# Kernel tuning notes

Hardware: AMD Instinct MI355X
Metric: run time of the kernel (lower is better)

## Reference

```python
import jax, jax.numpy as jnp
import numpy as np

B, N, D = 4, 1024, 1024   # batch, seq (x and context must match), model dim
H, DH = 16, 64            # heads, dim_head; inner_dim = H*DH = 1024
INNER = H * DH
EPS = 1e-5


def setup_inputs() -> dict:
    key = jax.random.key(0)
    ks = jax.random.split(key, 12)
    s = 0.02
    return {
        "x": jax.random.normal(ks[0], (B, N, D), dtype=jnp.float32),
        "context": jax.random.normal(ks[1], (B, N, D), dtype=jnp.float32),
        # weights stored as [in, out] (torch Linear weight transposed)
        "W_qk": jax.random.normal(ks[2], (D, INNER), dtype=jnp.float32) * s,
        "W_cqk": jax.random.normal(ks[3], (D, INNER), dtype=jnp.float32) * s,
        "W_v": jax.random.normal(ks[4], (D, INNER), dtype=jnp.float32) * s,
        "W_cv": jax.random.normal(ks[5], (D, INNER), dtype=jnp.float32) * s,
        "W_out": jax.random.normal(ks[6], (INNER, D), dtype=jnp.float32) * s,
        "b_out": jax.random.normal(ks[7], (D,), dtype=jnp.float32) * s,
        "W_cout": jax.random.normal(ks[8], (INNER, D), dtype=jnp.float32) * s,
        "b_cout": jax.random.normal(ks[9], (D,), dtype=jnp.float32) * s,
        "gamma": jnp.ones((D,), dtype=jnp.float32),
        "beta": jnp.zeros((D,), dtype=jnp.float32),
    }


def _split_heads(t):  # [b, n, h*d] -> [b, h, n, d]
    b, n, _ = t.shape
    return t.reshape(b, n, H, DH).transpose(0, 2, 1, 3)


def _merge_heads(t):  # [b, h, n, d] -> [b, n, h*d]
    b, h, n, d = t.shape
    return t.transpose(0, 2, 1, 3).reshape(b, n, h * d)


def _layernorm(y, gamma, beta):
    mu = jnp.mean(y, axis=-1, keepdims=True)
    var = jnp.var(y, axis=-1, keepdims=True)
    return gamma * (y - mu) * jax.lax.rsqrt(var + EPS) + beta


def reference(x, context, W_qk, W_cqk, W_v, W_cv, W_out, b_out, W_cout, b_cout, gamma, beta):
    scale = DH ** -0.5
    res = x + context                       # residual (requires identical shapes)
    # prenorm=False -> identity norms; dropout=0; talking_heads=False -> identity
    qk = _split_heads(x @ W_qk)             # [b,h,i,d]
    v = _split_heads(x @ W_v)               # [b,h,i,d]
    cqk = _split_heads(context @ W_cqk)     # [b,h,j,d]
    cv = _split_heads(context @ W_cv)       # [b,h,j,d]

    sim = jnp.einsum('bhid,bhjd->bhij', qk, cqk) * scale  # shared similarity
    attn = jax.nn.softmax(sim, axis=-1)      # row softmax (x attends to context)
    context_attn = jax.nn.softmax(sim, axis=-2)  # column softmax (context attends to x)

    out = jnp.einsum('bhij,bhjd->bhid', attn, cv)          # [b,h,i,d]
    context_out = jnp.einsum('bhji,bhjd->bhid', context_attn, v)  # [b,h,i,d]

    out = _merge_heads(out) @ W_out + b_out
    context_out = _merge_heads(context_out) @ W_cout + b_cout
    return _layernorm(out + context_out, gamma, beta) + res
```

## Files before the change

### kernel.cpp

```cpp
#include <hip/hip_runtime.h>
#include <hip/hip_bf16.h>

typedef unsigned short u16;
typedef __bf16 bf16x8 __attribute__((ext_vector_type(8)));
typedef float   f32x4 __attribute__((ext_vector_type(4)));
typedef u16     u16x8 __attribute__((ext_vector_type(8)));
typedef u16     u16x4 __attribute__((ext_vector_type(4)));

#define DEV static __device__ __forceinline__

DEV float bf2f(u16 b) { unsigned int u = ((unsigned int)b) << 16; return __builtin_bit_cast(float, u); }
DEV u16   f2bf(float f) { return __builtin_bit_cast(u16, (__bf16)f); }
DEV bf16x8 ldb(const u16* p) { return __builtin_bit_cast(bf16x8, *(const u16x8*)p); }

DEV f32x4 mfma_bf16(bf16x8 a, bf16x8 b, f32x4 c) {
  return __builtin_amdgcn_mfma_f32_16x16x32_bf16(a, b, c, 0, 0, 0);
}

DEV void gl16(const u16* g, u16* l) {
  __builtin_amdgcn_global_load_lds((const __attribute__((address_space(1))) unsigned int*)g,
                                   (__attribute__((address_space(3))) unsigned int*)l,
                                   16, 0, 0);
}

#define BAR_VM4() asm volatile("s_waitcnt vmcnt(4)\ns_barrier" ::: "memory")
#define BAR_VM0() asm volatile("s_waitcnt vmcnt(0)\ns_barrier" ::: "memory")
#define BAR_LG()  asm volatile("s_waitcnt lgkmcnt(0)\ns_barrier" ::: "memory")

__global__ __launch_bounds__(256) void detect_dtype(const u16* x, int* flag) {
  int tid = threadIdx.x;
  u16 lo = x[tid * 2];
  float v = bf2f(lo);
  float av = fabsf(v);
  bool plaus = (av > 1e-4f && av < 50.f);
  __shared__ int cnt;
  if (tid == 0) cnt = 0;
  __syncthreads();
  if (plaus) atomicAdd(&cnt, 1);
  __syncthreads();
  if (tid == 0) *flag = (cnt >= 128) ? 1 : 0;
}

struct Cv2 { const void* s[2]; u16* d[2]; };
__global__ __launch_bounds__(256) void convert_big(Cv2 p, const int* flagp) {
  int fl = *flagp;
  const void* src = p.s[blockIdx.z];
  u16* dst = p.d[blockIdx.z];
  size_t i = ((size_t)blockIdx.x * 256 + threadIdx.x) * 8;
  if (fl) {
    *(u16x8*)(dst + i) = *(const u16x8*)((const u16*)src + i);
  } else {
    const float* s = (const float*)src + i;
    u16x8 o;
#pragma unroll
    for (int k = 0; k < 8; ++k) o[k] = f2bf(s[k]);
    *(u16x8*)(dst + i) = o;
  }
}

struct Sm4 { const void* s[4]; u16* d[4]; };
__global__ __launch_bounds__(256) void convert_smalls(Sm4 p, const int* flagp) {
  int fl = *flagp;
  const void* src = p.s[blockIdx.x];
  u16* dst = p.d[blockIdx.x];
  int i = threadIdx.x * 4;
#pragma unroll
  for (int k = 0; k < 4; ++k)
    dst[i + k] = fl ? ((const u16*)src)[i + k] : f2bf(((const float*)src)[i + k]);
}

struct T6 { const void* s[6]; u16* d[6]; };

__global__ __launch_bounds__(256) void transpose6(T6 t, const int* flagp) {
  int fl = *flagp;
  __shared__ u16 tile[32][33];
  const void* src = t.s[blockIdx.z];
  u16* dst = t.d[blockIdx.z];
  int x0 = blockIdx.x * 32, y0 = blockIdx.y * 32;
  int tx = threadIdx.x & 31, ty = threadIdx.x >> 5;
#pragma unroll
  for (int i = 0; i < 32; i += 8) {
    size_t idx = (size_t)(y0 + ty + i) * 1024 + x0 + tx;
    tile[ty + i][tx] = fl ? ((const u16*)src)[idx] : f2bf(((const float*)src)[idx]);
  }
  __syncthreads();
#pragma unroll
  for (int i = 0; i < 32; i += 8)
    dst[(size_t)(x0 + ty + i) * 1024 + y0 + tx] = tile[tx][ty + i];
}

struct Proj4 { const u16* A[4]; const u16* Bt[4]; u16* C[4]; int mode[4]; };

__global__ __launch_bounds__(256) void gemm_proj(Proj4 p) {
  const int K = 1024, Nn = 1024;
  const u16* A  = p.A[blockIdx.z];
  const u16* Bt = p.Bt[blockIdx.z];
  u16* C = p.C[blockIdx.z];
  int mode = p.mode[blockIdx.z];

  __shared__ __align__(16) u16 As[2][128 * 32];
  __shared__ __align__(16) u16 Bs[2][128 * 32];

  int tid = threadIdx.x, lane = tid & 63, w = tid >> 6;
  int wm = w & 1, wn = w >> 1;
  int q4 = lane >> 4, c = lane & 15;

  int bid = blockIdx.y * 8 + blockIdx.x;
  int wg  = (bid & 7) * 32 + (bid >> 3);
  int m0 = (wg >> 3) * 128, n0 = (wg & 7) * 128;

  int r0 = w * 32 + (lane >> 2);
  int cc = (lane & 3) ^ ((lane >> 3) & 3);
  const u16* pA0 = A  + (size_t)(m0 + r0) * K + cc * 8;
  const u16* pB0 = Bt + (size_t)(n0 + r0) * K + cc * 8;
  int qs = (q4 ^ ((c >> 1) & 3)) * 8;

  f32x4 acc[4][4] = {};

#define STAGE_P(buf, koff)                                        \
  { gl16(pA0 + (koff),          As[buf] + w * 1024);              \
    gl16(pA0 + 16 * K + (koff), As[buf] + w * 1024 + 512);        \
    gl16(pB0 + (koff),          Bs[buf] + w * 1024);              \
    gl16(pB0 + 16 * K + (koff), Bs[buf] + w * 1024 + 512); }

#define COMP_P(buf)                                               \
  { bf16x8 af[4], bfr[4];                                         \
    _Pragma("unroll") for (int i = 0; i < 4; ++i)                 \
      af[i]  = ldb(As[buf] + (wm * 64 + i * 16 + c) * 32 + qs);   \
    _Pragma("unroll") for (int j = 0; j < 4; ++j)                 \
      bfr[j] = ldb(Bs[buf] + (wn * 64 + j * 16 + c) * 32 + qs);   \
    _Pragma("unroll") for (int i = 0; i < 4; ++i)                 \
      _Pragma("unroll") for (int j = 0; j < 4; ++j)               \
        acc[i][j] = mfma_bf16(af[i], bfr[j], acc[i][j]); }

  STAGE_P(0, 0);
  for (int t = 0; t < 30; t += 2) {
    STAGE_P(1, (t + 1) * 32);
    BAR_VM4();
    COMP_P(0);
    BAR_LG();
    STAGE_P(0, (t + 2) * 32);
    BAR_VM4();
    COMP_P(1);
    BAR_LG();
  }
  STAGE_P(1, 31 * 32);
  BAR_VM4();
  COMP_P(0);
  BAR_LG();
  BAR_VM0();
  COMP_P(1);
#undef STAGE_P
#undef COMP_P

  if (mode == 0) {
#pragma unroll
    for (int i = 0; i < 4; ++i) {
      int mrow = m0 + wm * 64 + i * 16 + q4 * 4;
#pragma unroll
      for (int j = 0; j < 4; ++j) {
        int col = n0 + wn * 64 + j * 16 + c;
#pragma unroll
        for (int r = 0; r < 4; ++r)
          C[(size_t)(mrow + r) * Nn + col] = f2bf(acc[i][j][r]);
      }
    }
  } else {
    int bidx = m0 >> 10;
#pragma unroll
    for (int i = 0; i < 4; ++i) {
      int mrow = m0 + wm * 64 + i * 16 + q4 * 4;
      int jj = mrow & 1023;
#pragma unroll
      for (int j = 0; j < 4; ++j) {
        int col = n0 + wn * 64 + j * 16 + c;
        int h = col >> 6, dh = col & 63;
        u16x4 pk;
#pragma unroll
        for (int r = 0; r < 4; ++r) pk[r] = f2bf(acc[i][j][r]);
        *(u16x4*)(C + ((size_t)((bidx * 16 + h) * 64 + dh)) * 1024 + jj) = pk;
      }
    }
  }
}

__global__ __launch_bounds__(256) void flash_attn(const u16* Q, const u16* Kg,
                                                  const u16* Vt, u16* O) {
  int bh = blockIdx.y; int b = bh >> 4, h = bh & 15;
  int i0 = blockIdx.x * 128;
  int tid = threadIdx.x, lane = tid & 63, w = tid >> 6;
  int q4 = lane >> 4, c = lane & 15;

  __shared__ __align__(16) u16 Ks[64 * 72];
  __shared__ __align__(16) u16 Vs[64 * 72];
  __shared__ __align__(16) u16 Ps[4][2][16 * 72];

  bf16x8 qf[2][2];
#pragma unroll
  for (int g = 0; g < 2; ++g) {
    const size_t qoff = ((size_t)(b * 1024 + i0 + g * 64 + w * 16 + c)) * 1024 + h * 64 + q4 * 8;
    qf[g][0] = ldb(Q + qoff);
    qf[g][1] = ldb(Q + qoff + 32);
  }

  f32x4 of[2][4] = {};
  f32x4 lacc[2] = {};
  bf16x8 ones;
#pragma unroll
  for (int k = 0; k < 8; ++k) ones[k] = (__bf16)1.0f;

  int jr = tid >> 2, seg = (tid & 3) * 16;
  const u16* krow_base = Kg + ((size_t)(b * 1024 + jr)) * 1024 + h * 64 + seg;
  const u16* vrow_base = Vt + ((size_t)((b * 16 + h) * 64 + jr)) * 1024 + seg;
  const float scale = 0.125f;

  u16x8 kv0 = *(const u16x8*)(krow_base);
  u16x8 kv1 = *(const u16x8*)(krow_base + 8);
  u16x8 vv0 = *(const u16x8*)(vrow_base);
  u16x8 vv1 = *(const u16x8*)(vrow_base + 8);

  for (int j0 = 0; j0 < 1024; j0 += 64) {
    __syncthreads();
    *(u16x8*)(Ks + jr * 72 + seg)     = kv0;
    *(u16x8*)(Ks + jr * 72 + seg + 8) = kv1;
    *(u16x8*)(Vs + jr * 72 + seg)     = vv0;
    *(u16x8*)(Vs + jr * 72 + seg + 8) = vv1;
    __syncthreads();

    if (j0 + 64 < 1024) {
      const u16* ks = krow_base + (size_t)(j0 + 64) * 1024;
      kv0 = *(const u16x8*)(ks);
      kv1 = *(const u16x8*)(ks + 8);
      const u16* vs = vrow_base + j0 + 64;
      vv0 = *(const u16x8*)(vs);
      vv1 = *(const u16x8*)(vs + 8);
    }

    f32x4 sf[2][4] = {};
    __builtin_amdgcn_s_setprio(1);
#pragma unroll
    for (int jc = 0; jc < 4; ++jc) {
      bf16x8 k0f = ldb(Ks + (jc * 16 + c) * 72 + q4 * 8);
      bf16x8 k1f = ldb(Ks + (jc * 16 + c) * 72 + 32 + q4 * 8);
#pragma unroll
      for (int g = 0; g < 2; ++g) {
        sf[g][jc] = mfma_bf16(k0f, qf[g][0], sf[g][jc]);
        sf[g][jc] = mfma_bf16(k1f, qf[g][1], sf[g][jc]);
      }
    }
    __builtin_amdgcn_s_setprio(0);

#pragma unroll
    for (int g = 0; g < 2; ++g)
#pragma unroll
      for (int jc = 0; jc < 4; ++jc) {
        u16x4 pk;
#pragma unroll
        for (int r = 0; r < 4; ++r) {
          float s = fminf(fmaxf(sf[g][jc][r] * scale, -60.f), 60.f);
          pk[r] = f2bf(__expf(s));
        }
        *(u16x4*)(Ps[w][g] + c * 72 + jc * 16 + q4 * 4) = pk;
      }

    asm volatile("s_waitcnt lgkmcnt(0)" ::: "memory");

    bf16x8 pf[2][2];
#pragma unroll
    for (int g = 0; g < 2; ++g) {
      pf[g][0] = ldb(Ps[w][g] + c * 72 + q4 * 8);
      pf[g][1] = ldb(Ps[w][g] + c * 72 + 32 + q4 * 8);
      lacc[g] = mfma_bf16(pf[g][0], ones, lacc[g]);
      lacc[g] = mfma_bf16(pf[g][1], ones, lacc[g]);
    }

    __builtin_amdgcn_s_setprio(1);
#pragma unroll
    for (int dc = 0; dc < 4; ++dc) {
      bf16x8 v0f = ldb(Vs + (dc * 16 + c) * 72 + q4 * 8);
      bf16x8 v1f = ldb(Vs + (dc * 16 + c) * 72 + 32 + q4 * 8);
#pragma unroll
      for (int g = 0; g < 2; ++g) {
        of[g][dc] = mfma_bf16(pf[g][0], v0f, of[g][dc]);
        of[g][dc] = mfma_bf16(pf[g][1], v1f, of[g][dc]);
      }
    }
    __builtin_amdgcn_s_setprio(0);
  }

#pragma unroll
  for (int g = 0; g < 2; ++g) {
    float inv[4];
#pragma unroll
    for (int r = 0; r < 4; ++r) inv[r] = 1.0f / lacc[g][r];
#pragma unroll
    for (int dc = 0; dc < 4; ++dc) {
      int col = h * 64 + dc * 16 + c;
#pragma unroll
      for (int r = 0; r < 4; ++r) {
        int irow = i0 + g * 64 + w * 16 + q4 * 4 + r;
        O[((size_t)(b * 1024 + irow)) * 1024 + col] = f2bf(of[g][dc][r] * inv[r]);
      }
    }
  }
}

__global__ __launch_bounds__(256) void gemm_final(const u16* A1, const u16* B1t,
                                                  const u16* A2, const u16* B2t,
                                                  const u16* b1, const u16* b2,
                                                  float* Y) {
  const int K = 1024, Nn = 1024;
  __shared__ __align__(16) u16 As[2][128 * 32];
  __shared__ __align__(16) u16 Bs[2][128 * 32];

  int tid = threadIdx.x, lane = tid & 63, w = tid >> 6;
  int wm = w & 1, wn = w >> 1;
  int q4 = lane >> 4, c = lane & 15;

  int bid = blockIdx.y * 8 + blockIdx.x;
  int wg  = (bid & 7) * 32 + (bid >> 3);
  int m0 = (wg >> 3) * 128, n0 = (wg & 7) * 128;

  int r0 = w * 32 + (lane >> 2);
  int cc = (lane & 3) ^ ((lane >> 3) & 3);
  const u16* A1p = A1  + (size_t)(m0 + r0) * K + cc * 8;
  const u16* A2p = A2  + (size_t)(m0 + r0) * K + cc * 8;
  const u16* B1p = B1t + (size_t)(n0 + r0) * K + cc * 8;
  const u16* B2p = B2t + (size_t)(n0 + r0) * K + cc * 8;
  int qs = (q4 ^ ((c >> 1) & 3)) * 8;

  f32x4 acc[4][4] = {};

#define STAGE_F(buf, kk)                                          \
  { const u16* Ap = ((kk) < 32) ? A1p : A2p;                      \
    const u16* Bp = ((kk) < 32) ? B1p : B2p;                      \
    int k0_ = ((kk) & 31) * 32;                                   \
    gl16(Ap + k0_,          As[buf] + w * 1024);                  \
    gl16(Ap + 16 * K + k0_, As[buf] + w * 1024 + 512);            \
    gl16(Bp + k0_,          Bs[buf] + w * 1024);                  \
    gl16(Bp + 16 * K + k0_, Bs[buf] + w * 1024 + 512); }

#define COMP_F(buf)                                               \
  { bf16x8 af[4], bfr[4];                                         \
    _Pragma("unroll") for (int i = 0; i < 4; ++i)                 \
      af[i]  = ldb(As[buf] + (wm * 64 + i * 16 + c) * 32 + qs);   \
    _Pragma("unroll") for (int j = 0; j < 4; ++j)                 \
      bfr[j] = ldb(Bs[buf] + (wn * 64 + j * 16 + c) * 32 + qs);   \
    _Pragma("unroll") for (int i = 0; i < 4; ++i)                 \
      _Pragma("unroll") for (int j = 0; j < 4; ++j)               \
        acc[i][j] = mfma_bf16(af[i], bfr[j], acc[i][j]); }

  STAGE_F(0, 0);
  for (int t = 0; t < 62; t += 2) {
    STAGE_F(1, t + 1);
    BAR_VM4();
    COMP_F(0);
    BAR_LG();
    STAGE_F(0, t + 2);
    BAR_VM4();
    COMP_F(1);
    BAR_LG();
  }
  STAGE_F(1, 63);
  BAR_VM4();
  COMP_F(0);
  BAR_LG();
  BAR_VM0();
  COMP_F(1);
#undef STAGE_F
#undef COMP_F

#pragma unroll
  for (int i = 0; i < 4; ++i) {
    int mrow = m0 + wm * 64 + i * 16 + q4 * 4;
#pragma unroll
    for (int j = 0; j < 4; ++j) {
      int col = n0 + wn * 64 + j * 16 + c;
      float bias = bf2f(b1[col]) + bf2f(b2[col]);
#pragma unroll
      for (int r = 0; r < 4; ++r)
        Y[(size_t)(mrow + r) * Nn + col] = acc[i][j][r] + bias;
    }
  }
}

__global__ __launch_bounds__(256) void ln_res(const float* Y, const u16* gamma, const u16* beta,
                                              const u16* x, const u16* ctx, void* out,
                                              const int* flagp) {
  int fl = *flagp;
  int row = blockIdx.x;
  int tid = threadIdx.x;
  const float* y = Y + (size_t)row * 1024;
  float4 v = *(const float4*)(y + tid * 4);
  float s  = v.x + v.y + v.z + v.w;
  float s2 = v.x * v.x + v.y * v.y + v.z * v.z + v.w * v.w;
#pragma unroll
  for (int off = 1; off < 64; off <<= 1) { s += __shfl_xor(s, off); s2 += __shfl_xor(s2, off); }
  __shared__ float red[8];
  int w = tid >> 6, lane = tid & 63;
  if (lane == 0) { red[w] = s; red[w + 4] = s2; }
  __syncthreads();
  float S  = red[0] + red[1] + red[2] + red[3];
  float S2 = red[4] + red[5] + red[6] + red[7];
  float mu  = S * (1.0f / 1024.0f);
  float var = S2 * (1.0f / 1024.0f) - mu * mu;
  float rs = rsqrtf(var + 1e-5f);
  size_t base = (size_t)row * 1024 + tid * 4;
  u16x4 gv = *(const u16x4*)(gamma + tid * 4);
  u16x4 bv = *(const u16x4*)(beta + tid * 4);
  u16x4 xv = *(const u16x4*)(x + base);
  u16x4 cv = *(const u16x4*)(ctx + base);
  float vv[4] = {v.x, v.y, v.z, v.w};
  float o[4];
#pragma unroll
  for (int k = 0; k < 4; ++k)
    o[k] = bf2f(gv[k]) * (vv[k] - mu) * rs + bf2f(bv[k]) + bf2f(xv[k]) + bf2f(cv[k]);
  if (fl) {
    u16x4 ov;
#pragma unroll
    for (int k = 0; k < 4; ++k) ov[k] = f2bf(o[k]);
    *(u16x4*)((u16*)out + base) = ov;
  } else {
    *(float4*)((float*)out + base) = make_float4(o[0], o[1], o[2], o[3]);
  }
}

__global__ __launch_bounds__(256) void sentinel(u16* out) {
  size_t i = ((size_t)blockIdx.x * 256 + threadIdx.x) * 8;
  u16 v = f2bf(12345.0f);
  u16x8 o = {v, v, v, v, v, v, v, v};
  *(u16x8*)(out + i) = o;
}

extern "C" void kernel_launch(void* const* d_in, const int* in_sizes, int n_in,
                              void* d_out, int out_size, void* d_ws, size_t ws_size,
                              hipStream_t stream) {
  (void)in_sizes; (void)n_in; (void)out_size;
  const size_t MB = 1024 * 1024;
  const size_t NEED = 61 * MB;
  if (ws_size < NEED) {
    sentinel<<<2048, 256, 0, stream>>>((u16*)d_out);
    return;
  }

  char* ws = (char*)d_ws;
  u16* wt[6];
  for (int i = 0; i < 6; ++i) wt[i] = (u16*)(ws + (size_t)i * 2 * MB);
  u16* xc   = (u16*)(ws + 12 * MB);
  u16* cc   = (u16*)(ws + 20 * MB);
  u16* qk   = (u16*)(ws + 28 * MB);
  u16* cqk  = (u16*)(ws + 36 * MB);
  u16* vt   = (u16*)(ws + 44 * MB);
  u16* cvt  = (u16*)(ws + 52 * MB);
  u16* oa   = (u16*)(ws + 0);
  u16* ca   = (u16*)(ws + 52 * MB);
  float* y  = (float*)(ws + 28 * MB);
  int* flag = (int*)(ws + 60 * MB);
  u16* b1c  = (u16*)(ws + 60 * MB + 4096);
  u16* b2c  = (u16*)(ws + 60 * MB + 8192);
  u16* gc   = (u16*)(ws + 60 * MB + 12288);
  u16* bc   = (u16*)(ws + 60 * MB + 16384);

  detect_dtype<<<1, 256, 0, stream>>>((const u16*)d_in[0], flag);

  Cv2 cv;
  cv.s[0] = d_in[0]; cv.d[0] = xc;
  cv.s[1] = d_in[1]; cv.d[1] = cc;
  convert_big<<<dim3(2048, 1, 2), 256, 0, stream>>>(cv, flag);

  Sm4 sm;
  sm.s[0] = d_in[7]; sm.d[0] = b1c;
  sm.s[1] = d_in[9]; sm.d[1] = b2c;
  sm.s[2] = d_in[10]; sm.d[2] = gc;
  sm.s[3] = d_in[11]; sm.d[3] = bc;
  convert_smalls<<<4, 256, 0, stream>>>(sm, flag);

  T6 t;
  t.s[0] = d_in[2]; t.d[0] = wt[0];
  t.s[1] = d_in[3]; t.d[1] = wt[1];
  t.s[2] = d_in[4]; t.d[2] = wt[2];
  t.s[3] = d_in[5]; t.d[3] = wt[3];
  t.s[4] = d_in[6]; t.d[4] = wt[4];
  t.s[5] = d_in[8]; t.d[5] = wt[5];
  transpose6<<<dim3(32, 32, 6), 256, 0, stream>>>(t, flag);

  Proj4 p;
  p.A[0] = xc; p.Bt[0] = wt[0]; p.C[0] = qk;  p.mode[0] = 0;
  p.A[1] = cc; p.Bt[1] = wt[1]; p.C[1] = cqk; p.mode[1] = 0;
  p.A[2] = xc; p.Bt[2] = wt[2]; p.C[2] = vt;  p.mode[2] = 1;
  p.A[3] = cc; p.Bt[3] = wt[3]; p.C[3] = cvt; p.mode[3] = 1;
  gemm_proj<<<dim3(8, 32, 4), 256, 0, stream>>>(p);

  flash_attn<<<dim3(8, 64), 256, 0, stream>>>(qk, cqk, cvt, oa);
  flash_attn<<<dim3(8, 64), 256, 0, stream>>>(cqk, qk, vt, ca);

  gemm_final<<<dim3(8, 32), 256, 0, stream>>>(oa, wt[4], ca, wt[5], b1c, b2c, y);

  ln_res<<<4096, 256, 0, stream>>>(y, gc, bc, xc, cc, d_out, flag);
}
```

Measured before the change: 281.7 us.

## Enlarge projection GEMM tiles, merge both attention launches, read residual from inputs

The projection GEMM goes from 128x128 tiles with K-step 32 and 256 threads to 256x256 tiles with K-step 64 and 512 threads, with a new XOR swizzle and raised MFMA priority. The goal is more operand reuse per LDS load and fewer barriers. The two flash-attention launches become one launch with a z-dimension of 2, so both directions can share the GPU at once. Because the two directions now run concurrently, the context-attention output buffer is moved so it no longer overlaps cvt, which the other direction still reads. The layernorm-residual kernel now reads x and context from the original inputs, since the converted copies are overwritten. The larger GEMM uses 128 KB of LDS and gives only 64 blocks per projection, which risks low occupancy and poor CU fill.

```diff
diff --git a/kernel.cpp b/kernel.cpp
--- a/kernel.cpp
+++ b/kernel.cpp
@@ -23,9 +23,10 @@
                                    16, 0, 0);
 }
 
-#define BAR_VM4() asm volatile("s_waitcnt vmcnt(4)\ns_barrier" ::: "memory")
-#define BAR_VM0() asm volatile("s_waitcnt vmcnt(0)\ns_barrier" ::: "memory")
-#define BAR_LG()  asm volatile("s_waitcnt lgkmcnt(0)\ns_barrier" ::: "memory")
+#define BAR_VM4()  asm volatile("s_waitcnt vmcnt(4)\ns_barrier" ::: "memory")
+#define BAR_VM0()  asm volatile("s_waitcnt vmcnt(0)\ns_barrier" ::: "memory")
+#define BAR_LG()   asm volatile("s_waitcnt lgkmcnt(0)\ns_barrier" ::: "memory")
+#define BAR_FULL() asm volatile("s_waitcnt vmcnt(0) lgkmcnt(0)\ns_barrier" ::: "memory")
 
 __global__ __launch_bounds__(256) void detect_dtype(const u16* x, int* flag) {
   int tid = threadIdx.x;
@@ -91,72 +92,82 @@
 
 struct Proj4 { const u16* A[4]; const u16* Bt[4]; u16* C[4]; int mode[4]; };
 
-__global__ __launch_bounds__(256) void gemm_proj(Proj4 p) {
+__global__ __launch_bounds__(512, 2) void gemm_proj(Proj4 p) {
   const int K = 1024, Nn = 1024;
   const u16* A  = p.A[blockIdx.z];
   const u16* Bt = p.Bt[blockIdx.z];
   u16* C = p.C[blockIdx.z];
   int mode = p.mode[blockIdx.z];
 
-  __shared__ __align__(16) u16 As[2][128 * 32];
-  __shared__ __align__(16) u16 Bs[2][128 * 32];
+  __shared__ __align__(16) u16 As[2][256 * 64];
+  __shared__ __align__(16) u16 Bs[2][256 * 64];
 
   int tid = threadIdx.x, lane = tid & 63, w = tid >> 6;
-  int wm = w & 1, wn = w >> 1;
+  int wm = w >> 2, wn = w & 3;
   int q4 = lane >> 4, c = lane & 15;
 
-  int bid = blockIdx.y * 8 + blockIdx.x;
-  int wg  = (bid & 7) * 32 + (bid >> 3);
-  int m0 = (wg >> 3) * 128, n0 = (wg & 7) * 128;
-
-  int r0 = w * 32 + (lane >> 2);
-  int cc = (lane & 3) ^ ((lane >> 3) & 3);
-  const u16* pA0 = A  + (size_t)(m0 + r0) * K + cc * 8;
-  const u16* pB0 = Bt + (size_t)(n0 + r0) * K + cc * 8;
-  int qs = (q4 ^ ((c >> 1) & 3)) * 8;
-
-  f32x4 acc[4][4] = {};
-
-#define STAGE_P(buf, koff)                                        \
-  { gl16(pA0 + (koff),          As[buf] + w * 1024);              \
-    gl16(pA0 + 16 * K + (koff), As[buf] + w * 1024 + 512);        \
-    gl16(pB0 + (koff),          Bs[buf] + w * 1024);              \
-    gl16(pB0 + 16 * K + (koff), Bs[buf] + w * 1024 + 512); }
-
-#define COMP_P(buf)                                               \
-  { bf16x8 af[4], bfr[4];                                         \
-    _Pragma("unroll") for (int i = 0; i < 4; ++i)                 \
-      af[i]  = ldb(As[buf] + (wm * 64 + i * 16 + c) * 32 + qs);   \
-    _Pragma("unroll") for (int j = 0; j < 4; ++j)                 \
-      bfr[j] = ldb(Bs[buf] + (wn * 64 + j * 16 + c) * 32 + qs);   \
-    _Pragma("unroll") for (int i = 0; i < 4; ++i)                 \
-      _Pragma("unroll") for (int j = 0; j < 4; ++j)               \
-        acc[i][j] = mfma_bf16(af[i], bfr[j], acc[i][j]); }
-
-  STAGE_P(0, 0);
-  for (int t = 0; t < 30; t += 2) {
-    STAGE_P(1, (t + 1) * 32);
-    BAR_VM4();
-    COMP_P(0);
-    BAR_LG();
-    STAGE_P(0, (t + 2) * 32);
-    BAR_VM4();
-    COMP_P(1);
-    BAR_LG();
-  }
-  STAGE_P(1, 31 * 32);
-  BAR_VM4();
-  COMP_P(0);
-  BAR_LG();
+  int bid = blockIdx.y * 4 + blockIdx.x;
+  int wg  = (bid & 7) * 8 + (bid >> 3);
+  int m0 = (wg >> 2) * 256, n0 = (wg & 3) * 256;
+
+  int srow = w * 8 + (lane >> 3);
+  int scol = ((lane & 7) ^ (lane >> 3)) * 8;
+  const u16* pAg = A  + (size_t)(m0 + srow) * K + scol;
+  const u16* pBg = Bt + (size_t)(n0 + srow) * K + scol;
+  int sdst = (w * 8) * 64;
+
+  int xo0 = ((0 * 4 + q4) ^ (c & 7)) * 8;
+  int xo1 = ((1 * 4 + q4) ^ (c & 7)) * 8;
+
+  f32x4 acc[8][4] = {};
+
+#define STAGE256(pb, kt)                                                    \
+  { int ko = (kt) * 64;                                                     \
+    _Pragma("unroll") for (int s = 0; s < 4; ++s) {                         \
+      gl16(pAg + (size_t)s * 64 * 1024 + ko, As[pb] + s * 4096 + sdst);     \
+      gl16(pBg + (size_t)s * 64 * 1024 + ko, Bs[pb] + s * 4096 + sdst);     \
+    } }
+
+#define COMP256(pb)                                                         \
+  { bf16x8 bq[4][2];                                                        \
+    _Pragma("unroll") for (int j = 0; j < 4; ++j) {                         \
+      int rb = (wn * 64 + j * 16 + c) * 64;                                 \
+      bq[j][0] = ldb(Bs[pb] + rb + xo0);                                    \
+      bq[j][1] = ldb(Bs[pb] + rb + xo1);                                    \
+    }                                                                       \
+    _Pragma("unroll") for (int f = 0; f < 4; ++f) {                         \
+      bf16x8 aq[2][2];                                                      \
+      _Pragma("unroll") for (int ii = 0; ii < 2; ++ii) {                    \
+        int ra = (wm * 128 + (f * 2 + ii) * 16 + c) * 64;                   \
+        aq[ii][0] = ldb(As[pb] + ra + xo0);                                 \
+        aq[ii][1] = ldb(As[pb] + ra + xo1);                                 \
+      }                                                                     \
+      __builtin_amdgcn_s_setprio(1);                                        \
+      _Pragma("unroll") for (int ii = 0; ii < 2; ++ii)                      \
+        _Pragma("unroll") for (int j = 0; j < 4; ++j) {                     \
+          acc[f*2+ii][j] = mfma_bf16(aq[ii][0], bq[j][0], acc[f*2+ii][j]);  \
+          acc[f*2+ii][j] = mfma_bf16(aq[ii][1], bq[j][1], acc[f*2+ii][j]);  \
+        }                                                                   \
+      __builtin_amdgcn_s_setprio(0);                                        \
+    } }
+
+  STAGE256(0, 0);
   BAR_VM0();
-  COMP_P(1);
-#undef STAGE_P
-#undef COMP_P
+  for (int t = 0; t < 16; t += 2) {
+    STAGE256(1, t + 1);
+    COMP256(0);
+    BAR_FULL();
+    if (t + 2 < 16) STAGE256(0, t + 2);
+    COMP256(1);
+    BAR_FULL();
+  }
+#undef STAGE256
+#undef COMP256
 
   if (mode == 0) {
 #pragma unroll
-    for (int i = 0; i < 4; ++i) {
-      int mrow = m0 + wm * 64 + i * 16 + q4 * 4;
+    for (int i = 0; i < 8; ++i) {
+      int mrow = m0 + wm * 128 + i * 16 + q4 * 4;
 #pragma unroll
       for (int j = 0; j < 4; ++j) {
         int col = n0 + wn * 64 + j * 16 + c;
@@ -168,8 +179,8 @@
   } else {
     int bidx = m0 >> 10;
 #pragma unroll
-    for (int i = 0; i < 4; ++i) {
-      int mrow = m0 + wm * 64 + i * 16 + q4 * 4;
+    for (int i = 0; i < 8; ++i) {
+      int mrow = m0 + wm * 128 + i * 16 + q4 * 4;
       int jj = mrow & 1023;
 #pragma unroll
       for (int j = 0; j < 4; ++j) {
@@ -184,8 +195,15 @@
   }
 }
 
-__global__ __launch_bounds__(256) void flash_attn(const u16* Q, const u16* Kg,
-                                                  const u16* Vt, u16* O) {
+struct FAz { const u16* Q[2]; const u16* Kp[2]; const u16* Vp[2]; u16* O[2]; };
+
+__global__ __launch_bounds__(256) void flash_attn(FAz fa) {
+  int z = blockIdx.z;
+  const u16* Q  = fa.Q[z];
+  const u16* Kg = fa.Kp[z];
+  const u16* Vt = fa.Vp[z];
+  u16* O = fa.O[z];
+
   int bh = blockIdx.y; int b = bh >> 4, h = bh & 15;
   int i0 = blockIdx.x * 128;
   int tid = threadIdx.x, lane = tid & 63, w = tid >> 6;
@@ -385,7 +403,7 @@
 }
 
 __global__ __launch_bounds__(256) void ln_res(const float* Y, const u16* gamma, const u16* beta,
-                                              const u16* x, const u16* ctx, void* out,
+                                              const void* x, const void* ctx, void* out,
                                               const int* flagp) {
   int fl = *flagp;
   int row = blockIdx.x;
@@ -408,13 +426,23 @@
   size_t base = (size_t)row * 1024 + tid * 4;
   u16x4 gv = *(const u16x4*)(gamma + tid * 4);
   u16x4 bv = *(const u16x4*)(beta + tid * 4);
-  u16x4 xv = *(const u16x4*)(x + base);
-  u16x4 cv = *(const u16x4*)(ctx + base);
+  float xr[4], cr[4];
+  if (fl) {
+    u16x4 xv = *(const u16x4*)((const u16*)x + base);
+    u16x4 cv = *(const u16x4*)((const u16*)ctx + base);
+#pragma unroll
+    for (int k = 0; k < 4; ++k) { xr[k] = bf2f(xv[k]); cr[k] = bf2f(cv[k]); }
+  } else {
+    float4 xv = *(const float4*)((const float*)x + base);
+    float4 cv = *(const float4*)((const float*)ctx + base);
+    xr[0] = xv.x; xr[1] = xv.y; xr[2] = xv.z; xr[3] = xv.w;
+    cr[0] = cv.x; cr[1] = cv.y; cr[2] = cv.z; cr[3] = cv.w;
+  }
   float vv[4] = {v.x, v.y, v.z, v.w};
   float o[4];
 #pragma unroll
   for (int k = 0; k < 4; ++k)
-    o[k] = bf2f(gv[k]) * (vv[k] - mu) * rs + bf2f(bv[k]) + bf2f(xv[k]) + bf2f(cv[k]);
+    o[k] = bf2f(gv[k]) * (vv[k] - mu) * rs + bf2f(bv[k]) + xr[k] + cr[k];
   if (fl) {
     u16x4 ov;
 #pragma unroll
@@ -453,7 +481,7 @@
   u16* vt   = (u16*)(ws + 44 * MB);
   u16* cvt  = (u16*)(ws + 52 * MB);
   u16* oa   = (u16*)(ws + 0);
-  u16* ca   = (u16*)(ws + 52 * MB);
+  u16* ca   = (u16*)(ws + 12 * MB);
   float* y  = (float*)(ws + 28 * MB);
   int* flag = (int*)(ws + 60 * MB);
   u16* b1c  = (u16*)(ws + 60 * MB + 4096);
@@ -489,12 +517,14 @@
   p.A[1] = cc; p.Bt[1] = wt[1]; p.C[1] = cqk; p.mode[1] = 0;
   p.A[2] = xc; p.Bt[2] = wt[2]; p.C[2] = vt;  p.mode[2] = 1;
   p.A[3] = cc; p.Bt[3] = wt[3]; p.C[3] = cvt; p.mode[3] = 1;
-  gemm_proj<<<dim3(8, 32, 4), 256, 0, stream>>>(p);
-
-  flash_attn<<<dim3(8, 64), 256, 0, stream>>>(qk, cqk, cvt, oa);
-  flash_attn<<<dim3(8, 64), 256, 0, stream>>>(cqk, qk, vt, ca);
+  gemm_proj<<<dim3(4, 16, 4), 512, 0, stream>>>(p);
+
+  FAz fa;
+  fa.Q[0] = qk;  fa.Kp[0] = cqk; fa.Vp[0] = cvt; fa.O[0] = oa;
+  fa.Q[1] = cqk; fa.Kp[1] = qk;  fa.Vp[1] = vt;  fa.O[1] = ca;
+  flash_attn<<<dim3(8, 64, 2), 256, 0, stream>>>(fa);
 
   gemm_final<<<dim3(8, 32), 256, 0, stream>>>(oa, wt[4], ca, wt[5], b1c, b2c, y);
 
-  ln_res<<<4096, 256, 0, stream>>>(y, gc, bc, xc, cc, d_out, flag);
-}
+  ln_res<<<4096, 256, 0, stream>>>(y, gc, bc, d_in[0], d_in[1], d_out, flag);
+}
```

New measurement: 268.0 us. 1.05x faster.
